# Kernel optimization log

Hardware: AMD Instinct MI355X
Metric: run time of the kernel (lower is better)

Reference implementation:

```python
import jax, jax.numpy as jnp
import numpy as np

T, N, D = 64, 40, 4
H, R, K = 256, 64, 2
E = N * (N - 1)


def _xavier(key, shape):
    std = (2.0 / (shape[0] + shape[1])) ** 0.5
    return (std * jax.random.normal(key, shape)).astype(jnp.float32)


def setup_inputs() -> dict:
    ks = iter(jax.random.split(jax.random.key(0), 40))
    send, recv = np.where(np.ones((N, N)) - np.eye(N))  # fully-connected directed graph, E = N*(N-1)
    p = {}
    p['inputs'] = jax.random.normal(next(ks), (1, T, N, D), dtype=jnp.float32)
    p['node_masks'] = jnp.ones((1, T, N), dtype=jnp.float32)
    p['send_edges'] = jnp.asarray(send, dtype=jnp.int32)
    p['recv_edges'] = jnp.asarray(recv, dtype=jnp.int32)
    for name, nin in (('mlp1', D), ('mlp2', 2 * H), ('mlp3', H), ('mlp4', 3 * H)):
        p[name + '_W1'] = _xavier(next(ks), (H, nin))
        p[name + '_b1'] = jnp.full((H,), 0.1, jnp.float32)
        p[name + '_W2'] = _xavier(next(ks), (H, H))
        p[name + '_b2'] = jnp.full((H,), 0.1, jnp.float32)
    s = float(1.0 / np.sqrt(R))
    for nm in ('fwd', 'rev'):
        p[nm + '_Wih'] = jax.random.uniform(next(ks), (4 * R, H), jnp.float32, -s, s)
        p[nm + '_Whh'] = jax.random.uniform(next(ks), (4 * R, R), jnp.float32, -s, s)
        p[nm + '_bih'] = jnp.zeros((4 * R,), jnp.float32)
        p[nm + '_bhh'] = jnp.zeros((4 * R,), jnp.float32)
    p['enc_W'] = _xavier(next(ks), (K, 2 * R))
    p['enc_b'] = jnp.full((K,), 0.1, jnp.float32)
    p['prior_W'] = _xavier(next(ks), (K, R))
    p['prior_b'] = jnp.full((K,), 0.1, jnp.float32)
    return p


def _mlp(x, W1, b1, W2, b2):
    # RefNRIMLP in eval mode with no_bn=True: elu(fc2(elu(fc1(x))))
    return jax.nn.elu(jax.nn.elu(x @ W1.T + b1) @ W2.T + b2)


def _lstm(xs, Wih, Whh, bih, bhh):
    # xs: [T, E, H] -> hidden states [T, E, R]; PyTorch LSTM gate order i, f, g, o
    def step(carry, xt):
        h, c = carry
        g = xt @ Wih.T + bih + h @ Whh.T + bhh
        i, f, gg, o = jnp.split(g, 4, axis=-1)
        c = jax.nn.sigmoid(f) * c + jax.nn.sigmoid(i) * jnp.tanh(gg)
        h = jax.nn.sigmoid(o) * jnp.tanh(c)
        return (h, c), h
    Rh = Whh.shape[1]
    init = (jnp.zeros((xs.shape[1], Rh), xs.dtype), jnp.zeros((xs.shape[1], Rh), xs.dtype))
    _, hs = jax.lax.scan(step, init, xs)
    return hs


def _encode(inputs, send, recv,
            m1W1, m1b1, m1W2, m1b2, m2W1, m2b1, m2W2, m2b2,
            m3W1, m3b1, m3W2, m3b2, m4W1, m4b1, m4W2, m4b2,
            fWih, fWhh, fbih, fbhh, rWih, rWhh, rbih, rbhh,
            encW, encb, priW, prib):
    x = inputs[0]                                                  # [T, N, D]
    h = _mlp(x, m1W1, m1b1, m1W2, m1b2)                            # [T, N, H]
    e = jnp.concatenate([h[:, send], h[:, recv]], axis=-1)         # node2edge gather [T, E, 2H]
    e = _mlp(e, m2W1, m2b1, m2W2, m2b2)                            # [T, E, H]
    skip = e
    n = jnp.zeros((x.shape[0], x.shape[1], e.shape[-1]), e.dtype)
    n = n.at[:, recv].add(e)                                       # edge2node scatter-add (index_add_)
    n = _mlp(n, m3W1, m3b1, m3W2, m3b2)                            # [T, N, H]
    e = jnp.concatenate([n[:, send], n[:, recv], skip], axis=-1)   # [T, E, 3H]
    e = _mlp(e, m4W1, m4b1, m4W2, m4b2)                            # per-edge features over time [T, E, H]
    fwd_h = _lstm(e, fWih, fWhh, fbih, fbhh)                       # [T, E, R]
    rev_h = _lstm(e[::-1], rWih, rWhh, rbih, rbhh)[::-1]           # [T, E, R]
    prior = fwd_h @ priW.T + prib                                  # [T, E, K]
    enc = jnp.concatenate([fwd_h, rev_h], axis=-1) @ encW.T + encb # [T, E, K]
    return jnp.concatenate([prior, enc], axis=-1)                  # [T, E, 2K]


def reference(inputs, node_masks, send_edges, recv_edges,
              mlp1_W1, mlp1_b1, mlp1_W2, mlp1_b2,
              mlp2_W1, mlp2_b1, mlp2_W2, mlp2_b2,
              mlp3_W1, mlp3_b1, mlp3_W2, mlp3_b2,
              mlp4_W1, mlp4_b1, mlp4_W2, mlp4_b2,
              fwd_Wih, fwd_Whh, fwd_bih, fwd_bhh,
              rev_Wih, rev_Whh, rev_bih, rev_bhh,
              enc_W, enc_b, prior_W, prior_b):
    del node_masks  # all nodes present -> static fully-connected graph each step
    return _encode(inputs, send_edges, recv_edges,
                   mlp1_W1, mlp1_b1, mlp1_W2, mlp1_b2,
                   mlp2_W1, mlp2_b1, mlp2_W2, mlp2_b2,
                   mlp3_W1, mlp3_b1, mlp3_W2, mlp3_b2,
                   mlp4_W1, mlp4_b1, mlp4_W2, mlp4_b2,
                   fwd_Wih, fwd_Whh, fwd_bih, fwd_bhh,
                   rev_Wih, rev_Whh, rev_bih, rev_bhh,
                   enc_W, enc_b, prior_W, prior_b)
```

## Files before the change

### kernel.cpp

```cpp
#include <hip/hip_runtime.h>
#include <math.h>

#define T_ 64
#define N_ 40
#define D_ 4
#define H_ 256
#define R_ 64
#define E_ 1560
#define TE_ (T_*E_)
#define TN_ (T_*N_)

typedef unsigned short us;
typedef short short8 __attribute__((ext_vector_type(8)));
typedef float f32x4 __attribute__((ext_vector_type(4)));

__device__ __forceinline__ float elu_f(float x){ return x > 0.f ? x : (__expf(x) - 1.f); }
__device__ __forceinline__ float sig_f(float x){ return 1.f/(1.f+__expf(-x)); }
__device__ __forceinline__ float tanh_f(float x){ return 2.f/(1.f+__expf(-2.f*x)) - 1.f; }
__device__ __forceinline__ float dot4(float4 a, float4 b){ return a.x*b.x + a.y*b.y + a.z*b.z + a.w*b.w; }

__device__ __forceinline__ float bf2f(us u){ return __uint_as_float(((unsigned int)u) << 16); }
__device__ __forceinline__ us f2bf(float f){
    unsigned int u = __float_as_uint(f);
    u += 0x7FFFu + ((u >> 16) & 1u);
    return (us)(u >> 16);
}
__device__ __forceinline__ float4 ld4f(const float* p){ return *(const float4*)p; }
__device__ __forceinline__ float4 ld4f(const us* p){
    ushort4 v = *(const ushort4*)p;
    return make_float4(bf2f(v.x), bf2f(v.y), bf2f(v.z), bf2f(v.w));
}
__device__ __forceinline__ void st4f(float* p, float4 v){ *(float4*)p = v; }
__device__ __forceinline__ void st4f(us* p, float4 v){
    ushort4 o; o.x = f2bf(v.x); o.y = f2bf(v.y); o.z = f2bf(v.z); o.w = f2bf(v.w);
    *(ushort4*)p = o;
}

__device__ __forceinline__ void gld16(void* lds, const void* g){
    __builtin_amdgcn_global_load_lds((const __attribute__((address_space(1))) unsigned int*)g,
                                     (__attribute__((address_space(3))) unsigned int*)lds,
                                     16, 0, 0);
}

__device__ __forceinline__ void wsplit1(const float* W, us* hi, us* lo, int i){
    const float w = W[i];
    const us h = f2bf(w);
    hi[i] = h;
    lo[i] = f2bf(w - bf2f(h));
}

__global__ __launch_bounds__(256)
void wsplit_all(const float* __restrict__ s0, us* h0, us* l0,
                const float* __restrict__ s1, us* h1, us* l1,
                const float* __restrict__ s2, us* h2, us* l2,
                const float* __restrict__ s3, us* h3, us* l3,
                const float* __restrict__ s4, us* h4, us* l4,
                const float* __restrict__ s5, us* h5, us* l5,
                const float* __restrict__ s6, us* h6, us* l6)
{
    int i = blockIdx.x * 256 + threadIdx.x;
    if (i < 65536) { wsplit1(s0, h0, l0, i); return; } i -= 65536;
    if (i < 65536) {
        const float w = s1[(i >> 8) * 768 + 512 + (i & 255)];
        const us h = f2bf(w);
        h1[i] = h;
        l1[i] = f2bf(w - bf2f(h));
        return;
    } i -= 65536;
    if (i < 65536) { wsplit1(s2, h2, l2, i); return; } i -= 65536;
    if (i < 65536) { wsplit1(s3, h3, l3, i); return; } i -= 65536;
    if (i < 65536) { wsplit1(s4, h4, l4, i); return; } i -= 65536;
    if (i < 16384) { wsplit1(s5, h5, l5, i); return; } i -= 16384;
    wsplit1(s6, h6, l6, i);
}

__global__ __launch_bounds__(256)
void mlp1_kernel(const float* __restrict__ x,
                 const float* __restrict__ W1, const float* __restrict__ b1,
                 const float* __restrict__ W2, const float* __restrict__ b2,
                 us* __restrict__ hout)
{
    __shared__ float xs[8][4];
    __shared__ float h1[8][256];
    const int tid = threadIdx.x;
    const int r0  = blockIdx.x * 8;

    if (tid < 32) xs[tid >> 2][tid & 3] = x[r0 * 4 + tid];
    __syncthreads();

    const float4 w1 = *(const float4*)&W1[tid * 4];
    const float bb1 = b1[tid];
    #pragma unroll
    for (int row = 0; row < 8; ++row) {
        float v = bb1 + xs[row][0]*w1.x + xs[row][1]*w1.y + xs[row][2]*w1.z + xs[row][3]*w1.w;
        h1[row][tid] = elu_f(v);
    }
    __syncthreads();

    float acc[8];
    const float bb2 = b2[tid];
    #pragma unroll
    for (int row = 0; row < 8; ++row) acc[row] = bb2;
    const float* w2row = W2 + (size_t)tid * 256;
    for (int k4 = 0; k4 < 64; ++k4) {
        const float4 w = *(const float4*)&w2row[k4 * 4];
        #pragma unroll
        for (int row = 0; row < 8; ++row) {
            const float4 hh = *(const float4*)&h1[row][k4 * 4];
            acc[row] += dot4(hh, w);
        }
    }
    #pragma unroll
    for (int row = 0; row < 8; ++row)
        hout[(size_t)(r0 + row) * 256 + tid] = f2bf(elu_f(acc[row]));
}

__global__ __launch_bounds__(256)
void node_proj(const us* __restrict__ A, const float* __restrict__ W,
               int wstride, float* __restrict__ P)
{
    __shared__ float As[16][64];
    __shared__ float Ws[16][64];

    const int tid  = threadIdx.x;
    const int am   = tid >> 2;
    const int gm   = blockIdx.x * 64 + am;
    const int part = blockIdx.y >> 2;
    const int wq   = blockIdx.y & 3;

    const us* aptr = A + (size_t)gm * 256;
    const float* wptr = W + (size_t)(wq * 64 + am) * wstride + part * 256;

    const int tx = tid & 15, ty = tid >> 4;
    float acc[4][4] = {};

    for (int k0 = 0; k0 < 256; k0 += 16) {
        const float4 a4 = ld4f(aptr + k0 + (tid & 3) * 4);
        const float4 w4 = *(const float4*)(wptr + k0 + (tid & 3) * 4);

        __syncthreads();
        const int ak = (tid & 3) * 4;
        As[ak+0][am] = a4.x; As[ak+1][am] = a4.y; As[ak+2][am] = a4.z; As[ak+3][am] = a4.w;
        Ws[ak+0][am] = w4.x; Ws[ak+1][am] = w4.y; Ws[ak+2][am] = w4.z; Ws[ak+3][am] = w4.w;
        __syncthreads();

        #pragma unroll
        for (int kq = 0; kq < 16; ++kq) {
            const float4 av = *(const float4*)&As[kq][ty * 4];
            const float4 wv = *(const float4*)&Ws[kq][tx * 4];
            const float a_[4] = {av.x, av.y, av.z, av.w};
            const float w_[4] = {wv.x, wv.y, wv.z, wv.w};
            #pragma unroll
            for (int i = 0; i < 4; ++i)
                #pragma unroll
                for (int j = 0; j < 4; ++j)
                    acc[i][j] += a_[i] * w_[j];
        }
    }

    const int gn = part * 256 + wq * 64 + tx * 4;
    #pragma unroll
    for (int i = 0; i < 4; ++i) {
        const int row = blockIdx.x * 64 + ty * 4 + i;
        float4 o;
        o.x = acc[i][0]; o.y = acc[i][1]; o.z = acc[i][2]; o.w = acc[i][3];
        *(float4*)(P + (size_t)row * 512 + gn) = o;
    }
}

__global__ __launch_bounds__(256)
void edge_gather_elu(const float* __restrict__ P, const float* __restrict__ b1,
                     const int* __restrict__ send, const int* __restrict__ recv,
                     us* __restrict__ out)
{
    const int tid = threadIdx.x;
    const int r   = blockIdx.x * 4 + (tid >> 6);
    const int c4  = (tid & 63) * 4;
    const int t = r / E_;
    const int e = r - t * E_;
    const float4 a  = *(const float4*)(P + ((size_t)(t * N_ + send[e])) * 512 + c4);
    const float4 b  = *(const float4*)(P + ((size_t)(t * N_ + recv[e])) * 512 + 256 + c4);
    const float4 bb = *(const float4*)(b1 + c4);
    float4 v;
    v.x = elu_f(a.x + b.x + bb.x);
    v.y = elu_f(a.y + b.y + bb.y);
    v.z = elu_f(a.z + b.z + bb.z);
    v.w = elu_f(a.w + b.w + bb.w);
    ushort4 o; o.x = f2bf(v.x); o.y = f2bf(v.y); o.z = f2bf(v.z); o.w = f2bf(v.w);
    *(ushort4*)(out + (size_t)r * 256 + c4) = o;
}

template<int MODE, bool DOELU>
__global__ __launch_bounds__(512, 2)
void gemm_mfma(const us* __restrict__ A,
               const us* __restrict__ Whi, const us* __restrict__ Wlo,
               const float* __restrict__ bias1, const float* __restrict__ bias2,
               const int* __restrict__ send, const int* __restrict__ recv,
               const float* __restrict__ Ptab,
               us* __restrict__ C, int Kdim,
               const us* __restrict__ Whi2, const us* __restrict__ Wlo2,
               const float* __restrict__ bias1b, const float* __restrict__ bias2b,
               us* __restrict__ C2)
{
    __shared__ char smem[98304];

    const int tid  = threadIdx.x;
    const int lane = tid & 63;
    const int w    = tid >> 6;
    const int ml   = lane & 15;
    const int q    = lane >> 4;
    const int bx   = blockIdx.x;

    if (MODE == 0 && C2 != nullptr && blockIdx.y == 1) {
        Whi = Whi2; Wlo = Wlo2; bias1 = bias1b; bias2 = bias2b; C = C2;
    }

    const int eh = w >> 2;
    const int fh = w & 3;

    const int lr   = lane >> 2;
    const int cofs = (((lane & 3) ^ ((lane >> 3) & 3)) * 8);

    const us *pA[2], *pWh[2], *pWl[2];
    #pragma unroll
    for (int i = 0; i < 2; ++i) {
        const int r = w * 32 + i * 16 + lr;
        pA[i]  = A   + (size_t)(bx * 256 + r) * Kdim;
        pWh[i] = Whi + (size_t)r * Kdim;
        pWl[i] = Wlo + (size_t)r * Kdim;
    }

    f32x4 acc[4][8];
    #pragma unroll
    for (int i = 0; i < 4; ++i)
        #pragma unroll
        for (int j = 0; j < 8; ++j)
            acc[i][j] = (f32x4){0.f, 0.f, 0.f, 0.f};

    auto stage = [&](int k0, char* base) {
        #pragma unroll
        for (int i = 0; i < 2; ++i) {
            gld16(base +         (w * 2 + i) * 1024, pA[i]  + k0 + cofs);
            gld16(base + 16384 + (w * 2 + i) * 1024, pWh[i] + k0 + cofs);
            gld16(base + 32768 + (w * 2 + i) * 1024, pWl[i] + k0 + cofs);
        }
    };

    const int qs16 = (q ^ ((ml >> 1) & 3)) * 16;

    stage(0, smem);
    const int nk = Kdim >> 5;
    for (int k = 0; k < nk; ++k) {
        char* cur = smem + (k & 1) * 49152;
        char* nxt = smem + ((k + 1) & 1) * 49152;
        __builtin_amdgcn_s_barrier();
        if (k + 1 < nk) {
            stage((k + 1) * 32, nxt);
            __builtin_amdgcn_s_waitcnt(0x3F76);
        } else {
            __builtin_amdgcn_s_waitcnt(0x3F70);
        }
        __builtin_amdgcn_s_barrier();

        short8 wh[4], wl[4], ef[8];
        #pragma unroll
        for (int mt = 0; mt < 4; ++mt) {
            const int blkOf = (fh * 4 + mt) * 1024 + ml * 64 + qs16;
            wh[mt] = *(const short8*)(cur + 16384 + blkOf);
            wl[mt] = *(const short8*)(cur + 32768 + blkOf);
        }
        #pragma unroll
        for (int nt = 0; nt < 8; ++nt) {
            const int blkOf = (eh * 8 + nt) * 1024 + ml * 64 + qs16;
            ef[nt] = *(const short8*)(cur + blkOf);
        }
        __builtin_amdgcn_s_setprio(1);
        #pragma unroll
        for (int nt = 0; nt < 8; ++nt)
            #pragma unroll
            for (int mt = 0; mt < 4; ++mt) {
                acc[mt][nt] = __builtin_amdgcn_mfma_f32_16x16x32_bf16(wh[mt], ef[nt], acc[mt][nt], 0, 0, 0);
                acc[mt][nt] = __builtin_amdgcn_mfma_f32_16x16x32_bf16(wl[mt], ef[nt], acc[mt][nt], 0, 0, 0);
            }
        __builtin_amdgcn_s_setprio(0);
    }

    int srowA[8], rrowA[8];
    if (MODE == 3) {
        #pragma unroll
        for (int nt = 0; nt < 8; ++nt) {
            const int row = bx * 256 + eh * 128 + nt * 16 + ml;
            const int t = row / E_;
            const int e = row - t * E_;
            srowA[nt] = t * N_ + send[e];
            rrowA[nt] = t * N_ + recv[e];
        }
    }

    #pragma unroll
    for (int mt = 0; mt < 4; ++mt) {
        const int colb = fh * 64 + mt * 16 + q * 4;
        float4 bb = *(const float4*)(bias1 + colb);
        if (bias2) {
            const float4 b2 = *(const float4*)(bias2 + colb);
            bb.x += b2.x; bb.y += b2.y; bb.z += b2.z; bb.w += b2.w;
        }
        #pragma unroll
        for (int nt = 0; nt < 8; ++nt) {
            const int row = bx * 256 + eh * 128 + nt * 16 + ml;
            float4 v;
            v.x = acc[mt][nt][0] + bb.x; v.y = acc[mt][nt][1] + bb.y;
            v.z = acc[mt][nt][2] + bb.z; v.w = acc[mt][nt][3] + bb.w;
            if (MODE == 3) {
                const float4 pS = *(const float4*)(Ptab + (size_t)srowA[nt] * 512 + colb);
                const float4 pR = *(const float4*)(Ptab + (size_t)rrowA[nt] * 512 + 256 + colb);
                v.x += pS.x + pR.x; v.y += pS.y + pR.y;
                v.z += pS.z + pR.z; v.w += pS.w + pR.w;
            }
            if (DOELU) { v.x = elu_f(v.x); v.y = elu_f(v.y); v.z = elu_f(v.z); v.w = elu_f(v.w); }
            ushort4 o; o.x = f2bf(v.x); o.y = f2bf(v.y); o.z = f2bf(v.z); o.w = f2bf(v.w);
            *(ushort4*)(C + (size_t)row * 256 + colb) = o;
        }
    }
}

template<bool DOELU, typename TA, typename TC>
__global__ __launch_bounds__(256)
void gemm_nt(const TA* __restrict__ A, const float* __restrict__ W,
             const float* __restrict__ bias1,
             TC* __restrict__ C, int M, int Kdim)
{
    __shared__ float As[16][64];
    __shared__ float Ws[16][64];

    const int tid = threadIdx.x;
    const int am  = tid >> 2;
    const int ak  = (tid & 3) * 4;
    const int gm  = blockIdx.x * 64 + am;

    const TA* aptr0 = A + (size_t)gm * Kdim;
    const float* wptr = W + (size_t)(blockIdx.y * 64 + am) * Kdim;

    const int tx = tid & 15, ty = tid >> 4;
    float acc[4][4] = {};

    for (int k0 = 0; k0 < Kdim; k0 += 16) {
        const float4 a4 = ld4f(aptr0 + k0 + ak);
        const float4 w4 = *(const float4*)(wptr + k0 + (tid & 3) * 4);

        __syncthreads();
        As[ak+0][am] = a4.x; As[ak+1][am] = a4.y; As[ak+2][am] = a4.z; As[ak+3][am] = a4.w;
        const int wk = (tid & 3) * 4;
        Ws[wk+0][am] = w4.x; Ws[wk+1][am] = w4.y; Ws[wk+2][am] = w4.z; Ws[wk+3][am] = w4.w;
        __syncthreads();

        #pragma unroll
        for (int kq = 0; kq < 16; ++kq) {
            const float4 av = *(const float4*)&As[kq][ty * 4];
            const float4 wv = *(const float4*)&Ws[kq][tx * 4];
            const float a_[4] = {av.x, av.y, av.z, av.w};
            const float w_[4] = {wv.x, wv.y, wv.z, wv.w};
            #pragma unroll
            for (int i = 0; i < 4; ++i)
                #pragma unroll
                for (int j = 0; j < 4; ++j)
                    acc[i][j] += a_[i] * w_[j];
        }
    }

    const int gn = blockIdx.y * 64 + tx * 4;
    const float4 bb = *(const float4*)&bias1[gn];
    #pragma unroll
    for (int i = 0; i < 4; ++i) {
        const int row = blockIdx.x * 64 + ty * 4 + i;
        float4 o;
        o.x = acc[i][0] + bb.x; o.y = acc[i][1] + bb.y;
        o.z = acc[i][2] + bb.z; o.w = acc[i][3] + bb.w;
        if (DOELU) { o.x = elu_f(o.x); o.y = elu_f(o.y); o.z = elu_f(o.z); o.w = elu_f(o.w); }
        st4f(C + (size_t)row * 256 + gn, o);
    }
}

__global__ __launch_bounds__(256)
void aggregate_kernel(const us* __restrict__ eSkip, const int* __restrict__ recv,
                      float* __restrict__ nAgg)
{
    const int t = blockIdx.x / N_;
    const int j = blockIdx.x - t * N_;
    const int c = threadIdx.x;
    const us* basep = eSkip + (size_t)t * E_ * H_ + c;
    float acc = 0.f;
    #pragma unroll
    for (int s = 0; s < N_; ++s) {
        if (s == j) continue;
        const int e = s * (N_ - 1) + (j < s ? j : j - 1);
        acc += bf2f(basep[(size_t)e * H_]);
    }
    nAgg[(size_t)blockIdx.x * H_ + c] = acc;
}

__global__ __launch_bounds__(256)
void lstm_mfma(const us* __restrict__ Gf, const us* __restrict__ Gr,
               const us* __restrict__ fWhhH, const us* __restrict__ fWhhL,
               const us* __restrict__ rWhhH, const us* __restrict__ rWhhL,
               float* __restrict__ hsF, float* __restrict__ hsR)
{
    const int NBD = (E_ + 15) / 16;
    const bool revd = (int)blockIdx.x >= NBD;
    const int blk = revd ? (int)blockIdx.x - NBD : (int)blockIdx.x;
    const int e0 = blk * 16;
    const us* G  = revd ? Gr : Gf;
    const us* WH = revd ? rWhhH : fWhhH;
    const us* WL = revd ? rWhhL : fWhhL;
    float* hs    = revd ? hsR : hsF;

    const int tid  = threadIdx.x;
    const int lane = tid & 63;
    const int w    = tid >> 6;
    const int ml   = lane & 15;
    const int q    = lane >> 4;

    __shared__ us hHi[2][16][72];
    __shared__ us hLo[2][16][72];

    short8 wfh[4][2], wfl[4][2];
    #pragma unroll
    for (int mt = 0; mt < 4; ++mt) {
        const int row = mt * 64 + w * 16 + ml;
        #pragma unroll
        for (int ks = 0; ks < 2; ++ks) {
            wfh[mt][ks] = *(const short8*)(WH + (size_t)row * 64 + ks * 32 + q * 8);
            wfl[mt][ks] = *(const short8*)(WL + (size_t)row * 64 + ks * 32 + q * 8);
        }
    }

    for (int i = tid; i < 16 * 72; i += 256) { (&hHi[0][0][0])[i] = 0; (&hLo[0][0][0])[i] = 0; }

    const int eMF = min(e0 + ml, E_ - 1);
    const bool wr = (e0 + ml) < E_;
    const int gOfs = w * 16 + q * 4;
    float4 cst = make_float4(0.f, 0.f, 0.f, 0.f);

    ushort4 gcur[4], gnxt[4];
    {
        const int tt0 = revd ? (T_ - 1) : 0;
        const us* gp = G + ((size_t)tt0 * E_ + eMF) * 256 + gOfs;
        #pragma unroll
        for (int mt = 0; mt < 4; ++mt) gcur[mt] = *(const ushort4*)(gp + mt * 64);
    }
    __syncthreads();

    for (int s = 0; s < T_; ++s) {
        const int tt = revd ? (T_ - 1 - s) : s;
        {
            const int sn = (s + 1 < T_) ? s + 1 : s;
            const int tn = revd ? (T_ - 1 - sn) : sn;
            const us* gp = G + ((size_t)tn * E_ + eMF) * 256 + gOfs;
            #pragma unroll
            for (int mt = 0; mt < 4; ++mt) gnxt[mt] = *(const ushort4*)(gp + mt * 64);
        }
        const int rb = s & 1, wb = rb ^ 1;
        short8 bh[2], bl[2];
        #pragma unroll
        for (int ks = 0; ks < 2; ++ks) {
            bh[ks] = *(const short8*)(&hHi[rb][ml][ks * 32 + q * 8]);
            bl[ks] = *(const short8*)(&hLo[rb][ml][ks * 32 + q * 8]);
        }
        f32x4 acc[4];
        #pragma unroll
        for (int mt = 0; mt < 4; ++mt) {
            acc[mt][0] = bf2f(gcur[mt].x); acc[mt][1] = bf2f(gcur[mt].y);
            acc[mt][2] = bf2f(gcur[mt].z); acc[mt][3] = bf2f(gcur[mt].w);
            #pragma unroll
            for (int ks = 0; ks < 2; ++ks) {
                acc[mt] = __builtin_amdgcn_mfma_f32_16x16x32_bf16(wfh[mt][ks], bh[ks], acc[mt], 0, 0, 0);
                acc[mt] = __builtin_amdgcn_mfma_f32_16x16x32_bf16(wfh[mt][ks], bl[ks], acc[mt], 0, 0, 0);
                acc[mt] = __builtin_amdgcn_mfma_f32_16x16x32_bf16(wfl[mt][ks], bh[ks], acc[mt], 0, 0, 0);
            }
        }
        float4 hv;
        cst.x = sig_f(acc[1][0])*cst.x + sig_f(acc[0][0])*tanh_f(acc[2][0]); hv.x = sig_f(acc[3][0])*tanh_f(cst.x);
        cst.y = sig_f(acc[1][1])*cst.y + sig_f(acc[0][1])*tanh_f(acc[2][1]); hv.y = sig_f(acc[3][1])*tanh_f(cst.y);
        cst.z = sig_f(acc[1][2])*cst.z + sig_f(acc[0][2])*tanh_f(acc[2][2]); hv.z = sig_f(acc[3][2])*tanh_f(cst.z);
        cst.w = sig_f(acc[1][3])*cst.w + sig_f(acc[0][3])*tanh_f(acc[2][3]); hv.w = sig_f(acc[3][3])*tanh_f(cst.w);
        ushort4 hh4, hl4;
        hh4.x = f2bf(hv.x); hl4.x = f2bf(hv.x - bf2f(hh4.x));
        hh4.y = f2bf(hv.y); hl4.y = f2bf(hv.y - bf2f(hh4.y));
        hh4.z = f2bf(hv.z); hl4.z = f2bf(hv.z - bf2f(hh4.z));
        hh4.w = f2bf(hv.w); hl4.w = f2bf(hv.w - bf2f(hh4.w));
        *(ushort4*)(&hHi[wb][ml][gOfs]) = hh4;
        *(ushort4*)(&hLo[wb][ml][gOfs]) = hl4;
        if (wr)
            *(float4*)(&hs[((size_t)tt * E_ + e0 + ml) * 64 + gOfs]) = hv;
        __syncthreads();
        #pragma unroll
        for (int mt = 0; mt < 4; ++mt) gcur[mt] = gnxt[mt];
    }
}

__global__ __launch_bounds__(256)
void out_kernel(const float* __restrict__ hsF, const float* __restrict__ hsR,
                const float* __restrict__ priW, const float* __restrict__ prib,
                const float* __restrict__ encW, const float* __restrict__ encb,
                float* __restrict__ out)
{
    const int idx = blockIdx.x * 256 + threadIdx.x;
    const float* f = hsF + (size_t)idx * 64;
    const float* r = hsR + (size_t)idx * 64;
    float p0 = prib[0], p1 = prib[1], q0 = encb[0], q1 = encb[1];
    #pragma unroll
    for (int k4 = 0; k4 < 16; ++k4) {
        const float4 fv = *(const float4*)(f + k4 * 4);
        const float4 rv = *(const float4*)(r + k4 * 4);
        p0 += dot4(fv, *(const float4*)(priW + k4 * 4));
        p1 += dot4(fv, *(const float4*)(priW + 64 + k4 * 4));
        q0 += dot4(fv, *(const float4*)(encW + k4 * 4))
            + dot4(rv, *(const float4*)(encW + 64 + k4 * 4));
        q1 += dot4(fv, *(const float4*)(encW + 128 + k4 * 4))
            + dot4(rv, *(const float4*)(encW + 192 + k4 * 4));
    }
    float4 o; o.x = p0; o.y = p1; o.z = q0; o.w = q1;
    *(float4*)(out + (size_t)idx * 4) = o;
}

extern "C" void kernel_launch(void* const* d_in, const int* in_sizes, int n_in,
                              void* d_out, int out_size, void* d_ws, size_t ws_size,
                              hipStream_t stream)
{
    const float* x    = (const float*)d_in[0];
    const int*   send = (const int*)d_in[2];
    const int*   recv = (const int*)d_in[3];
    const float* m1W1 = (const float*)d_in[4];  const float* m1b1 = (const float*)d_in[5];
    const float* m1W2 = (const float*)d_in[6];  const float* m1b2 = (const float*)d_in[7];
    const float* m2W1 = (const float*)d_in[8];  const float* m2b1 = (const float*)d_in[9];
    const float* m2W2 = (const float*)d_in[10]; const float* m2b2 = (const float*)d_in[11];
    const float* m3W1 = (const float*)d_in[12]; const float* m3b1 = (const float*)d_in[13];
    const float* m3W2 = (const float*)d_in[14]; const float* m3b2 = (const float*)d_in[15];
    const float* m4W1 = (const float*)d_in[16]; const float* m4b1 = (const float*)d_in[17];
    const float* m4W2 = (const float*)d_in[18]; const float* m4b2 = (const float*)d_in[19];
    const float* fWih = (const float*)d_in[20]; const float* fWhh = (const float*)d_in[21];
    const float* fbih = (const float*)d_in[22]; const float* fbhh = (const float*)d_in[23];
    const float* rWih = (const float*)d_in[24]; const float* rWhh = (const float*)d_in[25];
    const float* rbih = (const float*)d_in[26]; const float* rbhh = (const float*)d_in[27];
    const float* encW = (const float*)d_in[28]; const float* encb = (const float*)d_in[29];
    const float* priW = (const float*)d_in[30]; const float* prib = (const float*)d_in[31];

    const size_t SZN  = (size_t)TN_ * H_;
    const size_t SZE  = (size_t)TE_ * H_;
    float* n_agg = (float*)d_ws;
    float* m3t   = n_agg + SZN;
    float* Ptab  = (float*)d_ws;
    us* h16      = (us*)(m3t + SZN);
    us* n3       = h16 + SZN;
    us* w2bH = n3  + SZN;          us* w2bL = w2bH + 65536;
    us* w4aH = w2bL + 65536;       us* w4aL = w4aH + 65536;
    us* w4bH = w4aL + 65536;       us* w4bL = w4bH + 65536;
    us* wfiH = w4bL + 65536;       us* wfiL = wfiH + 65536;
    us* wriH = wfiL + 65536;       us* wriL = wriH + 65536;
    us* whfH = wriL + 65536;       us* whfL = whfH + 16384;
    us* whrH = whfL + 16384;       us* whrL = whrH + 16384;
    us* bufA16 = whrL + 16384;
    us* bufB16 = bufA16 + SZE;
    us* bufC16 = bufB16 + SZE;
    float* hsF = (float*)bufC16;
    float* hsR = hsF + (size_t)TE_ * R_;
    const size_t needed = ((size_t)(bufC16 + SZE) - (size_t)d_ws);
    if (ws_size < needed) return;

    const dim3 gMF(TE_ / 256, 1), gMFd(TE_ / 256, 2), gN(TN_ / 64, 4), gNP(TN_ / 64, 8);
    const us* z = nullptr; const float* zf = nullptr; us* zo = nullptr;

    wsplit_all<<<1408, 256, 0, stream>>>(m2W2, w2bH, w2bL,
                                         m4W1, w4aH, w4aL,
                                         m4W2, w4bH, w4bL,
                                         fWih, wfiH, wfiL, rWih, wriH, wriL,
                                         fWhh, whfH, whfL, rWhh, whrH, whrL);

    mlp1_kernel<<<TN_ / 8, 256, 0, stream>>>(x, m1W1, m1b1, m1W2, m1b2, h16);
    node_proj<<<gNP, 256, 0, stream>>>(h16, m2W1, 512, Ptab);
    edge_gather_elu<<<TE_ / 4, 256, 0, stream>>>(Ptab, m2b1, send, recv, bufA16);
    gemm_mfma<0, true><<<gMF, 512, 0, stream>>>(bufA16, w2bH, w2bL, m2b2, nullptr, send, recv, zf, bufB16, 256, z, z, zf, zf, zo);
    aggregate_kernel<<<TN_, 256, 0, stream>>>(bufB16, recv, n_agg);
    gemm_nt<true, float, float><<<gN, 256, 0, stream>>>(n_agg, m3W1, m3b1, m3t, TN_, 256);
    gemm_nt<true, float, us><<<gN, 256, 0, stream>>>(m3t, m3W2, m3b2, n3, TN_, 256);
    node_proj<<<gNP, 256, 0, stream>>>(n3, m4W1, 768, Ptab);
    gemm_mfma<3, true><<<gMF, 512, 0, stream>>>(bufB16, w4aH, w4aL, m4b1, nullptr, send, recv, Ptab, bufA16, 256, z, z, zf, zf, zo);
    gemm_mfma<0, true><<<gMF, 512, 0, stream>>>(bufA16, w4bH, w4bL, m4b2, nullptr, send, recv, zf, bufC16, 256, z, z, zf, zf, zo);
    gemm_mfma<0, false><<<gMFd, 512, 0, stream>>>(bufC16, wfiH, wfiL, fbih, fbhh, send, recv, zf, bufA16, 256,
                                                  wriH, wriL, rbih, rbhh, bufB16);
    lstm_mfma<<<2 * ((E_ + 15) / 16), 256, 0, stream>>>(bufA16, bufB16, whfH, whfL, whrH, whrL, hsF, hsR);
    out_kernel<<<TE_ / 256, 256, 0, stream>>>(hsF, hsR, priW, prib, encW, encb, (float*)d_out);
}
```

Baseline: 586.2 us.

## Fuse mlp4 and LSTM input-projection GEMM chain into one LDS-resident kernel

Replaces the generic double-buffered gemm_mfma with a 128-row-tile kernel. Each block holds its whole bf16 activation tile in LDS, and each wave streams its own slice of weight columns. The mlp4 fc1 (with the gathered node-projection add), fc2, and the forward and reverse LSTM input projections are chained in one kernel. Intermediate activations are written back into LDS instead of global memory, which removes several full edge-tensor round trips and kernel launches. In exchange, occupancy drops to one 128KB-LDS block per CU, and weights are re-read from L2 per block for each of the four stages.

```diff
diff --git a/kernel.cpp b/kernel.cpp
--- a/kernel.cpp
+++ b/kernel.cpp
@@ -190,136 +190,278 @@
     *(ushort4*)(out + (size_t)r * 256 + c4) = o;
 }
 
-template<int MODE, bool DOELU>
-__global__ __launch_bounds__(512, 2)
-void gemm_mfma(const us* __restrict__ A,
-               const us* __restrict__ Whi, const us* __restrict__ Wlo,
-               const float* __restrict__ bias1, const float* __restrict__ bias2,
-               const int* __restrict__ send, const int* __restrict__ recv,
-               const float* __restrict__ Ptab,
-               us* __restrict__ C, int Kdim,
-               const us* __restrict__ Whi2, const us* __restrict__ Wlo2,
-               const float* __restrict__ bias1b, const float* __restrict__ bias2b,
-               us* __restrict__ C2)
-{
-    __shared__ char smem[98304];
-
-    const int tid  = threadIdx.x;
-    const int lane = tid & 63;
-    const int w    = tid >> 6;
-    const int ml   = lane & 15;
-    const int q    = lane >> 4;
-    const int bx   = blockIdx.x;
-
-    if (MODE == 0 && C2 != nullptr && blockIdx.y == 1) {
-        Whi = Whi2; Wlo = Wlo2; bias1 = bias1b; bias2 = bias2b; C = C2;
-    }
-
-    const int eh = w >> 2;
-    const int fh = w & 3;
-
-    const int lr   = lane >> 2;
+#define LGKM0 0xC07F
+#define VM0   0x3F70
+#define VM4   0x3F74
+
+__global__ __launch_bounds__(512, 1)
+void gemm_bf(const us* __restrict__ A, const us* __restrict__ WH, const us* __restrict__ WL,
+             const float* __restrict__ bias, us* __restrict__ C)
+{
+    __shared__ char smem[131072];
+    char* AG = smem;
+    char* WS = smem + 65536;
+
+    const int tid = threadIdx.x, lane = tid & 63, w = tid >> 6;
+    const int ml = lane & 15, q = lane >> 4;
+    const int lr = lane >> 2;
     const int cofs = (((lane & 3) ^ ((lane >> 3) & 3)) * 8);
-
-    const us *pA[2], *pWh[2], *pWl[2];
-    #pragma unroll
-    for (int i = 0; i < 2; ++i) {
-        const int r = w * 32 + i * 16 + lr;
-        pA[i]  = A   + (size_t)(bx * 256 + r) * Kdim;
-        pWh[i] = Whi + (size_t)r * Kdim;
-        pWl[i] = Wlo + (size_t)r * Kdim;
-    }
-
-    f32x4 acc[4][8];
-    #pragma unroll
-    for (int i = 0; i < 4; ++i)
-        #pragma unroll
-        for (int j = 0; j < 8; ++j)
-            acc[i][j] = (f32x4){0.f, 0.f, 0.f, 0.f};
-
-    auto stage = [&](int k0, char* base) {
-        #pragma unroll
-        for (int i = 0; i < 2; ++i) {
-            gld16(base +         (w * 2 + i) * 1024, pA[i]  + k0 + cofs);
-            gld16(base + 16384 + (w * 2 + i) * 1024, pWh[i] + k0 + cofs);
-            gld16(base + 32768 + (w * 2 + i) * 1024, pWl[i] + k0 + cofs);
-        }
-    };
-
     const int qs16 = (q ^ ((ml >> 1) & 3)) * 16;
-
-    stage(0, smem);
-    const int nk = Kdim >> 5;
-    for (int k = 0; k < nk; ++k) {
-        char* cur = smem + (k & 1) * 49152;
-        char* nxt = smem + ((k + 1) & 1) * 49152;
-        __builtin_amdgcn_s_barrier();
-        if (k + 1 < nk) {
-            stage((k + 1) * 32, nxt);
-            __builtin_amdgcn_s_waitcnt(0x3F76);
+    const int bx = blockIdx.x;
+
+    char* myWS = WS + w * 8192;
+    const size_t wrow0 = (size_t)((w * 2 + 0) * 16 + lr) * 256 + cofs;
+    const size_t wrow1 = (size_t)((w * 2 + 1) * 16 + lr) * 256 + cofs;
+
+    #pragma unroll
+    for (int g = 0; g < 8; ++g)
+        gld16(AG + w * 8192 + g * 1024,
+              A + (size_t)(bx * 128 + g * 16 + lr) * 256 + w * 32 + cofs);
+    __builtin_amdgcn_s_waitcnt(VM0);
+    __syncthreads();
+
+    f32x4 acc[2][8];
+    #pragma unroll
+    for (int mt = 0; mt < 2; ++mt)
+        #pragma unroll
+        for (int nt = 0; nt < 8; ++nt) acc[mt][nt] = (f32x4){0.f,0.f,0.f,0.f};
+
+    gld16(myWS +    0, WH + wrow0);
+    gld16(myWS + 1024, WH + wrow1);
+    gld16(myWS + 2048, WL + wrow0);
+    gld16(myWS + 3072, WL + wrow1);
+
+    for (int k = 0; k < 8; ++k) {
+        char* cur = myWS + (k & 1) * 4096;
+        char* nxt = myWS + ((k + 1) & 1) * 4096;
+        if (k < 7) {
+            const int k0 = (k + 1) * 32;
+            gld16(nxt,        WH + wrow0 + k0);
+            gld16(nxt + 1024, WH + wrow1 + k0);
+            gld16(nxt + 2048, WL + wrow0 + k0);
+            gld16(nxt + 3072, WL + wrow1 + k0);
+            __builtin_amdgcn_s_waitcnt(VM4);
         } else {
-            __builtin_amdgcn_s_waitcnt(0x3F70);
-        }
-        __builtin_amdgcn_s_barrier();
-
-        short8 wh[4], wl[4], ef[8];
-        #pragma unroll
-        for (int mt = 0; mt < 4; ++mt) {
-            const int blkOf = (fh * 4 + mt) * 1024 + ml * 64 + qs16;
-            wh[mt] = *(const short8*)(cur + 16384 + blkOf);
-            wl[mt] = *(const short8*)(cur + 32768 + blkOf);
-        }
-        #pragma unroll
-        for (int nt = 0; nt < 8; ++nt) {
-            const int blkOf = (eh * 8 + nt) * 1024 + ml * 64 + qs16;
-            ef[nt] = *(const short8*)(cur + blkOf);
-        }
+            __builtin_amdgcn_s_waitcnt(VM0);
+        }
+        __builtin_amdgcn_sched_barrier(0);
+        short8 wh[2], wl[2], ef[8];
+        wh[0] = *(const short8*)(cur +        ml*64 + qs16);
+        wh[1] = *(const short8*)(cur + 1024 + ml*64 + qs16);
+        wl[0] = *(const short8*)(cur + 2048 + ml*64 + qs16);
+        wl[1] = *(const short8*)(cur + 3072 + ml*64 + qs16);
+        #pragma unroll
+        for (int nt = 0; nt < 8; ++nt)
+            ef[nt] = *(const short8*)(AG + k*8192 + nt*1024 + ml*64 + qs16);
         __builtin_amdgcn_s_setprio(1);
         #pragma unroll
         for (int nt = 0; nt < 8; ++nt)
             #pragma unroll
-            for (int mt = 0; mt < 4; ++mt) {
-                acc[mt][nt] = __builtin_amdgcn_mfma_f32_16x16x32_bf16(wh[mt], ef[nt], acc[mt][nt], 0, 0, 0);
-                acc[mt][nt] = __builtin_amdgcn_mfma_f32_16x16x32_bf16(wl[mt], ef[nt], acc[mt][nt], 0, 0, 0);
+            for (int mt = 0; mt < 2; ++mt) {
+                acc[mt][nt] = __builtin_amdgcn_mfma_f32_16x16x32_bf16(wh[mt], ef[nt], acc[mt][nt], 0,0,0);
+                acc[mt][nt] = __builtin_amdgcn_mfma_f32_16x16x32_bf16(wl[mt], ef[nt], acc[mt][nt], 0,0,0);
             }
         __builtin_amdgcn_s_setprio(0);
-    }
-
-    int srowA[8], rrowA[8];
-    if (MODE == 3) {
+        __builtin_amdgcn_s_waitcnt(LGKM0);
+        __builtin_amdgcn_sched_barrier(0);
+    }
+
+    #pragma unroll
+    for (int mt = 0; mt < 2; ++mt) {
+        const int col = w * 32 + mt * 16 + q * 4;
+        const float4 bb = *(const float4*)(bias + col);
         #pragma unroll
         for (int nt = 0; nt < 8; ++nt) {
-            const int row = bx * 256 + eh * 128 + nt * 16 + ml;
+            const int row = bx * 128 + nt * 16 + ml;
+            float4 v;
+            v.x = elu_f(acc[mt][nt][0] + bb.x); v.y = elu_f(acc[mt][nt][1] + bb.y);
+            v.z = elu_f(acc[mt][nt][2] + bb.z); v.w = elu_f(acc[mt][nt][3] + bb.w);
+            ushort4 o; o.x = f2bf(v.x); o.y = f2bf(v.y); o.z = f2bf(v.z); o.w = f2bf(v.w);
+            *(ushort4*)(C + (size_t)row * 256 + col) = o;
+        }
+    }
+}
+
+__global__ __launch_bounds__(512, 1)
+void fused_m4(const us* __restrict__ Askip,
+              const us* __restrict__ w4aH, const us* __restrict__ w4aL, const float* __restrict__ m4b1,
+              const us* __restrict__ w4bH, const us* __restrict__ w4bL, const float* __restrict__ m4b2,
+              const us* __restrict__ wfiH, const us* __restrict__ wfiL,
+              const float* __restrict__ fbih, const float* __restrict__ fbhh,
+              const us* __restrict__ wriH, const us* __restrict__ wriL,
+              const float* __restrict__ rbih, const float* __restrict__ rbhh,
+              const float* __restrict__ Ptab, const int* __restrict__ send, const int* __restrict__ recv,
+              us* __restrict__ Gf, us* __restrict__ Gr)
+{
+    __shared__ char smem[131072];
+    char* AG = smem;
+    char* WS = smem + 65536;
+
+    const int tid = threadIdx.x, lane = tid & 63, w = tid >> 6;
+    const int ml = lane & 15, q = lane >> 4;
+    const int lr = lane >> 2;
+    const int cofs = (((lane & 3) ^ ((lane >> 3) & 3)) * 8);
+    const int qs16 = (q ^ ((ml >> 1) & 3)) * 16;
+    const int bx = blockIdx.x;
+
+    char* myWS = WS + w * 8192;
+    const size_t wrow0 = (size_t)((w * 2 + 0) * 16 + lr) * 256 + cofs;
+    const size_t wrow1 = (size_t)((w * 2 + 1) * 16 + lr) * 256 + cofs;
+
+    int gtOf[2];
+    #pragma unroll
+    for (int mt = 0; mt < 2; ++mt)
+        gtOf[mt] = w * 8192 + ml * 64 + (((mt * 2 + (q >> 1)) ^ ((ml >> 1) & 3)) * 16) + (q & 1) * 8;
+
+    f32x4 acc[2][8];
+
+    auto runUnit = [&](const us* WH, const us* WL) {
+        #pragma unroll
+        for (int mt = 0; mt < 2; ++mt)
+            #pragma unroll
+            for (int nt = 0; nt < 8; ++nt) acc[mt][nt] = (f32x4){0.f,0.f,0.f,0.f};
+        gld16(myWS +    0, WH + wrow0);
+        gld16(myWS + 1024, WH + wrow1);
+        gld16(myWS + 2048, WL + wrow0);
+        gld16(myWS + 3072, WL + wrow1);
+        for (int k = 0; k < 8; ++k) {
+            char* cur = myWS + (k & 1) * 4096;
+            char* nxt = myWS + ((k + 1) & 1) * 4096;
+            if (k < 7) {
+                const int k0 = (k + 1) * 32;
+                gld16(nxt,        WH + wrow0 + k0);
+                gld16(nxt + 1024, WH + wrow1 + k0);
+                gld16(nxt + 2048, WL + wrow0 + k0);
+                gld16(nxt + 3072, WL + wrow1 + k0);
+                __builtin_amdgcn_s_waitcnt(VM4);
+            } else {
+                __builtin_amdgcn_s_waitcnt(VM0);
+            }
+            __builtin_amdgcn_sched_barrier(0);
+            short8 wh[2], wl[2], ef[8];
+            wh[0] = *(const short8*)(cur +        ml*64 + qs16);
+            wh[1] = *(const short8*)(cur + 1024 + ml*64 + qs16);
+            wl[0] = *(const short8*)(cur + 2048 + ml*64 + qs16);
+            wl[1] = *(const short8*)(cur + 3072 + ml*64 + qs16);
+            #pragma unroll
+            for (int nt = 0; nt < 8; ++nt)
+                ef[nt] = *(const short8*)(AG + k*8192 + nt*1024 + ml*64 + qs16);
+            __builtin_amdgcn_s_setprio(1);
+            #pragma unroll
+            for (int nt = 0; nt < 8; ++nt)
+                #pragma unroll
+                for (int mt = 0; mt < 2; ++mt) {
+                    acc[mt][nt] = __builtin_amdgcn_mfma_f32_16x16x32_bf16(wh[mt], ef[nt], acc[mt][nt], 0,0,0);
+                    acc[mt][nt] = __builtin_amdgcn_mfma_f32_16x16x32_bf16(wl[mt], ef[nt], acc[mt][nt], 0,0,0);
+                }
+            __builtin_amdgcn_s_setprio(0);
+            __builtin_amdgcn_s_waitcnt(LGKM0);
+            __builtin_amdgcn_sched_barrier(0);
+        }
+    };
+
+    #pragma unroll
+    for (int g = 0; g < 8; ++g)
+        gld16(AG + w * 8192 + g * 1024,
+              Askip + (size_t)(bx * 128 + g * 16 + lr) * 256 + w * 32 + cofs);
+    __builtin_amdgcn_s_waitcnt(VM0);
+    __syncthreads();
+
+    ushort4 r16[2][8];
+
+    runUnit(w4aH, w4aL);
+    {
+        int srw[8], rrw[8];
+        #pragma unroll
+        for (int nt = 0; nt < 8; ++nt) {
+            const int row = bx * 128 + nt * 16 + ml;
             const int t = row / E_;
             const int e = row - t * E_;
-            srowA[nt] = t * N_ + send[e];
-            rrowA[nt] = t * N_ + recv[e];
-        }
-    }
-
-    #pragma unroll
-    for (int mt = 0; mt < 4; ++mt) {
-        const int colb = fh * 64 + mt * 16 + q * 4;
-        float4 bb = *(const float4*)(bias1 + colb);
-        if (bias2) {
-            const float4 b2 = *(const float4*)(bias2 + colb);
-            bb.x += b2.x; bb.y += b2.y; bb.z += b2.z; bb.w += b2.w;
-        }
+            srw[nt] = t * N_ + send[e];
+            rrw[nt] = t * N_ + recv[e];
+        }
+        #pragma unroll
+        for (int mt = 0; mt < 2; ++mt) {
+            const int col = w * 32 + mt * 16 + q * 4;
+            const float4 bb = *(const float4*)(m4b1 + col);
+            #pragma unroll
+            for (int nt = 0; nt < 8; ++nt) {
+                float4 v;
+                v.x = acc[mt][nt][0] + bb.x; v.y = acc[mt][nt][1] + bb.y;
+                v.z = acc[mt][nt][2] + bb.z; v.w = acc[mt][nt][3] + bb.w;
+                const float4 pS = *(const float4*)(Ptab + (size_t)srw[nt] * 512 + col);
+                const float4 pR = *(const float4*)(Ptab + (size_t)rrw[nt] * 512 + 256 + col);
+                v.x += pS.x + pR.x; v.y += pS.y + pR.y;
+                v.z += pS.z + pR.z; v.w += pS.w + pR.w;
+                v.x = elu_f(v.x); v.y = elu_f(v.y); v.z = elu_f(v.z); v.w = elu_f(v.w);
+                ushort4 o; o.x = f2bf(v.x); o.y = f2bf(v.y); o.z = f2bf(v.z); o.w = f2bf(v.w);
+                r16[mt][nt] = o;
+            }
+        }
+    }
+    __syncthreads();
+    #pragma unroll
+    for (int mt = 0; mt < 2; ++mt)
+        #pragma unroll
+        for (int nt = 0; nt < 8; ++nt)
+            *(ushort4*)(AG + gtOf[mt] + nt * 1024) = r16[mt][nt];
+    __syncthreads();
+
+    runUnit(w4bH, w4bL);
+    #pragma unroll
+    for (int mt = 0; mt < 2; ++mt) {
+        const int col = w * 32 + mt * 16 + q * 4;
+        const float4 bb = *(const float4*)(m4b2 + col);
         #pragma unroll
         for (int nt = 0; nt < 8; ++nt) {
-            const int row = bx * 256 + eh * 128 + nt * 16 + ml;
+            float4 v;
+            v.x = elu_f(acc[mt][nt][0] + bb.x); v.y = elu_f(acc[mt][nt][1] + bb.y);
+            v.z = elu_f(acc[mt][nt][2] + bb.z); v.w = elu_f(acc[mt][nt][3] + bb.w);
+            ushort4 o; o.x = f2bf(v.x); o.y = f2bf(v.y); o.z = f2bf(v.z); o.w = f2bf(v.w);
+            r16[mt][nt] = o;
+        }
+    }
+    __syncthreads();
+    #pragma unroll
+    for (int mt = 0; mt < 2; ++mt)
+        #pragma unroll
+        for (int nt = 0; nt < 8; ++nt)
+            *(ushort4*)(AG + gtOf[mt] + nt * 1024) = r16[mt][nt];
+    __syncthreads();
+
+    runUnit(wfiH, wfiL);
+    #pragma unroll
+    for (int mt = 0; mt < 2; ++mt) {
+        const int col = w * 32 + mt * 16 + q * 4;
+        float4 bb = *(const float4*)(fbih + col);
+        const float4 b2 = *(const float4*)(fbhh + col);
+        bb.x += b2.x; bb.y += b2.y; bb.z += b2.z; bb.w += b2.w;
+        #pragma unroll
+        for (int nt = 0; nt < 8; ++nt) {
+            const int row = bx * 128 + nt * 16 + ml;
             float4 v;
             v.x = acc[mt][nt][0] + bb.x; v.y = acc[mt][nt][1] + bb.y;
             v.z = acc[mt][nt][2] + bb.z; v.w = acc[mt][nt][3] + bb.w;
-            if (MODE == 3) {
-                const float4 pS = *(const float4*)(Ptab + (size_t)srowA[nt] * 512 + colb);
-                const float4 pR = *(const float4*)(Ptab + (size_t)rrowA[nt] * 512 + 256 + colb);
-                v.x += pS.x + pR.x; v.y += pS.y + pR.y;
-                v.z += pS.z + pR.z; v.w += pS.w + pR.w;
-            }
-            if (DOELU) { v.x = elu_f(v.x); v.y = elu_f(v.y); v.z = elu_f(v.z); v.w = elu_f(v.w); }
             ushort4 o; o.x = f2bf(v.x); o.y = f2bf(v.y); o.z = f2bf(v.z); o.w = f2bf(v.w);
-            *(ushort4*)(C + (size_t)row * 256 + colb) = o;
+            *(ushort4*)(Gf + (size_t)row * 256 + col) = o;
+        }
+    }
+
+    runUnit(wriH, wriL);
+    #pragma unroll
+    for (int mt = 0; mt < 2; ++mt) {
+        const int col = w * 32 + mt * 16 + q * 4;
+        float4 bb = *(const float4*)(rbih + col);
+        const float4 b2 = *(const float4*)(rbhh + col);
+        bb.x += b2.x; bb.y += b2.y; bb.z += b2.z; bb.w += b2.w;
+        #pragma unroll
+        for (int nt = 0; nt < 8; ++nt) {
+            const int row = bx * 128 + nt * 16 + ml;
+            float4 v;
+            v.x = acc[mt][nt][0] + bb.x; v.y = acc[mt][nt][1] + bb.y;
+            v.z = acc[mt][nt][2] + bb.z; v.w = acc[mt][nt][3] + bb.w;
+            ushort4 o; o.x = f2bf(v.x); o.y = f2bf(v.y); o.z = f2bf(v.z); o.w = f2bf(v.w);
+            *(ushort4*)(Gr + (size_t)row * 256 + col) = o;
         }
     }
 }
@@ -567,8 +709,7 @@
     const size_t needed = ((size_t)(bufC16 + SZE) - (size_t)d_ws);
     if (ws_size < needed) return;
 
-    const dim3 gMF(TE_ / 256, 1), gMFd(TE_ / 256, 2), gN(TN_ / 64, 4), gNP(TN_ / 64, 8);
-    const us* z = nullptr; const float* zf = nullptr; us* zo = nullptr;
+    const dim3 gN(TN_ / 64, 4), gNP(TN_ / 64, 8);
 
     wsplit_all<<<1408, 256, 0, stream>>>(m2W2, w2bH, w2bL,
                                          m4W1, w4aH, w4aL,
@@ -579,15 +720,17 @@
     mlp1_kernel<<<TN_ / 8, 256, 0, stream>>>(x, m1W1, m1b1, m1W2, m1b2, h16);
     node_proj<<<gNP, 256, 0, stream>>>(h16, m2W1, 512, Ptab);
     edge_gather_elu<<<TE_ / 4, 256, 0, stream>>>(Ptab, m2b1, send, recv, bufA16);
-    gemm_mfma<0, true><<<gMF, 512, 0, stream>>>(bufA16, w2bH, w2bL, m2b2, nullptr, send, recv, zf, bufB16, 256, z, z, zf, zf, zo);
+    gemm_bf<<<TE_ / 128, 512, 0, stream>>>(bufA16, w2bH, w2bL, m2b2, bufB16);
     aggregate_kernel<<<TN_, 256, 0, stream>>>(bufB16, recv, n_agg);
     gemm_nt<true, float, float><<<gN, 256, 0, stream>>>(n_agg, m3W1, m3b1, m3t, TN_, 256);
     gemm_nt<true, float, us><<<gN, 256, 0, stream>>>(m3t, m3W2, m3b2, n3, TN_, 256);
     node_proj<<<gNP, 256, 0, stream>>>(n3, m4W1, 768, Ptab);
-    gemm_mfma<3, true><<<gMF, 512, 0, stream>>>(bufB16, w4aH, w4aL, m4b1, nullptr, send, recv, Ptab, bufA16, 256, z, z, zf, zf, zo);
-    gemm_mfma<0, true><<<gMF, 512, 0, stream>>>(bufA16, w4bH, w4bL, m4b2, nullptr, send, recv, zf, bufC16, 256, z, z, zf, zf, zo);
-    gemm_mfma<0, false><<<gMFd, 512, 0, stream>>>(bufC16, wfiH, wfiL, fbih, fbhh, send, recv, zf, bufA16, 256,
-                                                  wriH, wriL, rbih, rbhh, bufB16);
+    fused_m4<<<TE_ / 128, 512, 0, stream>>>(bufB16,
+                                            w4aH, w4aL, m4b1,
+                                            w4bH, w4bL, m4b2,
+                                            wfiH, wfiL, fbih, fbhh,
+                                            wriH, wriL, rbih, rbhh,
+                                            Ptab, send, recv, bufA16, bufB16);
     lstm_mfma<<<2 * ((E_ + 15) / 16), 256, 0, stream>>>(bufA16, bufB16, whfH, whfL, whrH, whrL, hsF, hsR);
     out_kernel<<<TE_ / 256, 256, 0, stream>>>(hsF, hsR, priW, prib, encW, encb, (float*)d_out);
 }
```

After: 547.9 us. -6.5%, faster.
